# Performance work log

Hardware: AMD Instinct MI355X
Metric: run time of the kernel (lower is better)

## Reference

```python
import jax, jax.numpy as jnp
import numpy as np
from jax import lax

N, K = 4, 8
B, C, H, W = 16, 64, 256, 256


def setup_inputs() -> dict:
    key = jax.random.key(0)
    k1, k2, k3 = jax.random.split(key, 3)
    x = jax.random.normal(k1, (B, C, H, W), dtype=jnp.float32)
    z = jax.random.normal(k2, (B, C, N * K, N * K), dtype=jnp.float32)
    # torch init is ones; perturb slightly so the FFT filtering is non-trivial
    freq_coeff = 1.0 + 0.1 * jax.random.normal(k3, (K, K // 2 + 1, 2), dtype=jnp.float32)
    return {"x": x, "z": z, "freq_coeff": freq_coeff}


def _get_feature_weights(z, freq_coeff, n, k):
    b, c = z.shape[0], z.shape[1]
    # [b,c,n,k,n,k] -> [b,n,n,c,k,k] -> [b*n*n, c, k, k]
    w1 = z.reshape(b, c, n, k, n, k).transpose(0, 2, 4, 1, 3, 5).reshape(b * n * n, c, k, k)
    f = jnp.fft.rfft2(w1, norm="ortho")  # [b*n*n, c, k, k//2+1] complex
    # torch.rfft(..)*freq_coeff multiplies real/imag parts by separate real coeffs
    f_new = f.real * freq_coeff[..., 0] + 1j * (f.imag * freq_coeff[..., 1])
    return jnp.fft.irfft2(f_new, s=(k, k), norm="ortho")  # [b*n*n, c, k, k]


def _grouped_conv(data, weight, b):
    # data: [1, b*c, h, w], weight: [b*n*n, c, k, k], groups=b, stride 2, VALID
    return lax.conv_general_dilated(
        data, weight, window_strides=(2, 2), padding="VALID",
        dimension_numbers=("NCHW", "OIHW", "NCHW"), feature_group_count=b)


def reference(x, z, freq_coeff):
    k = freq_coeff.shape[0]
    n = z.shape[2] // k
    b, c, h, w = x.shape
    weight = _get_feature_weights(z, freq_coeff, n, k)
    data = x.reshape(1, b * c, h, w)
    resp = _grouped_conv(data, weight, b)  # [1, b*n*n, h', w']
    norm = _grouped_conv(data * data, jnp.ones_like(weight), b)
    norm = norm + jnp.std(norm, ddof=1) / 10 + 1e-9
    norm = lax.stop_gradient(0.01 / jnp.sqrt(norm))
    resp = resp * norm
    _, cc, hh, ww = resp.shape
    return resp.reshape(b, cc // b, hh, ww)
```

## Files before the change

### kernel.cpp

```cpp
#include <hip/hip_runtime.h>

typedef short short8 __attribute__((ext_vector_type(8)));
typedef float f32x4 __attribute__((ext_vector_type(4)));
typedef unsigned int uint4v __attribute__((ext_vector_type(4)));

static constexpr int OHW = 125;
static constexpr int PLN = OHW * OHW;

__device__ inline unsigned int bf16_rne(float f) {
  unsigned int u = __float_as_uint(f);
  return (u + 0x7FFFu + ((u >> 16) & 1u)) >> 16;
}

__global__ __launch_bounds__(256) void fft_mat_kernel(
    const float* __restrict__ fc, float* __restrict__ Mt, double* __restrict__ red) {
  if (blockIdx.x == 0 && threadIdx.x < 2) red[threadIdx.x] = 0.0;
  int e = blockIdx.x * 256 + threadIdx.x;
  int uv = e >> 6, xy = e & 63;
  int u = uv >> 3, v = uv & 7, xx = xy >> 3, yy = xy & 7;
  const float R2 = 0.70710678118654752f;
  const float ct[8] = {1.f, R2, 0.f, -R2, -1.f, -R2, 0.f, R2};
  const float st[8] = {0.f, R2, 1.f, R2, 0.f, -R2, -1.f, -R2};
  float sumv = 0.f;
  #pragma unroll
  for (int p = 0; p < 8; ++p) {
    #pragma unroll
    for (int q = 0; q < 8; ++q) {
      float Re, Im;
      if (q <= 4) {
        int th = (p * u + q * v) & 7;
        float a = fc[(p * 5 + q) * 2 + 0];
        float b = fc[(p * 5 + q) * 2 + 1];
        Re = a * ct[th];
        Im = -b * st[th];
      } else {
        int pp = (8 - p) & 7, qq = 8 - q;
        int th = (pp * u + qq * v) & 7;
        float a = fc[(pp * 5 + qq) * 2 + 0];
        float b = fc[(pp * 5 + qq) * 2 + 1];
        Re = a * ct[th];
        Im = b * st[th];
      }
      int ph = (p * xx + q * yy) & 7;
      sumv += Re * ct[ph] - Im * st[ph];
    }
  }
  Mt[e] = sumv * (1.0f / 64.0f);
}

__global__ __launch_bounds__(256) void weight_kernel(
    const float* __restrict__ z, const float* __restrict__ Mt,
    unsigned short* __restrict__ Wq) {
  int blk = blockIdx.x;
  int G = blk >> 2, cq = blk & 3;
  int b = G >> 4, n1 = (G >> 2) & 3, n2 = G & 3;
  int oc = G & 15;
  int tid = threadIdx.x;
  int cs = tid >> 6, xy = tid & 63;
  __shared__ float Ms[4096];
  __shared__ float zb[4][64];
  for (int i = tid; i < 4096; i += 256) Ms[i] = Mt[i];
  for (int it = 0; it < 4; ++it) {
    int c = cq * 16 + cs * 4 + it;
    __syncthreads();
    int u = xy >> 3, vv = xy & 7;
    zb[cs][xy] = z[(size_t)(b * 64 + c) * 1024 + (n1 * 8 + u) * 32 + (n2 * 8 + vv)];
    __syncthreads();
    float acc = 0.f;
    #pragma unroll
    for (int i = 0; i < 64; ++i) acc += Ms[i * 64 + xy] * zb[cs][i];
    Wq[((size_t)(b * 64 + c) * 16 + oc) * 64 + xy] = (unsigned short)bf16_rne(acc);
  }
}

__global__ __launch_bounds__(256) void conv_fused_kernel(
    const float* __restrict__ x, const unsigned short* __restrict__ Wq,
    float* __restrict__ resp, float* __restrict__ plane, double* __restrict__ red) {
  __shared__ unsigned int ldsx[2016];
  const int g = blockIdx.x, iblk = blockIdx.y, jh = blockIdx.z;
  const int i0 = iblk * 4;
  const int tid = threadIdx.x;
  const int lane = tid & 63, ri = tid >> 6;
  const int q = lane >> 4, n = lane & 15;

  const float* xg = x + (size_t)g * 64 * 65536;
  const unsigned short* wgc = Wq + (size_t)g * 65536;

  int it_goff[2], it_l[2];
  bool it_act[2];
  #pragma unroll
  for (int s = 0; s < 2; ++s) {
    int item = tid + (s << 8);
    int row = item / 36, c4 = item - row * 36;
    it_act[s] = row < 14;
    int rabs = 2 * i0 + row; if (rabs > 255) rabs = 255;
    int cabs = 128 * jh + 4 * c4; if (cabs > 252) cabs = 252;
    it_goff[s] = rabs * 256 + cabs;
    it_l[s] = row * 72 + 2 * c4;
  }
  const int aoff0 = n * 64 + q * 8;
  int dbase[2];
  #pragma unroll
  for (int h = 0; h < 2; ++h)
    dbase[h] = (2 * ri + q + 4 * h) * 72 + n;

  f32x4 acc[4];
  #pragma unroll
  for (int t = 0; t < 4; ++t) acc[t] = (f32x4){0.f, 0.f, 0.f, 0.f};
  float racc[2][2] = {{0.f, 0.f}, {0.f, 0.f}};

  f32x4 xv[2];
  short8 a_cur[2], a_nxt[2];

  #pragma unroll
  for (int s = 0; s < 2; ++s) xv[s] = *(const f32x4*)(xg + it_goff[s]);
  #pragma unroll
  for (int h = 0; h < 2; ++h)
    a_cur[h] = *(const short8*)(wgc + aoff0 + 32 * h);
  #pragma unroll
  for (int s = 0; s < 2; ++s) {
    if (it_act[s]) {
      racc[s][0] += xv[s][0] * xv[s][0] + xv[s][1] * xv[s][1];
      racc[s][1] += xv[s][2] * xv[s][2] + xv[s][3] * xv[s][3];
      unsigned int p0 = bf16_rne(xv[s][0]) | (bf16_rne(xv[s][1]) << 16);
      unsigned int p1 = bf16_rne(xv[s][2]) | (bf16_rne(xv[s][3]) << 16);
      ldsx[it_l[s]] = p0;
      ldsx[it_l[s] + 1] = p1;
    }
  }
  #pragma unroll
  for (int s = 0; s < 2; ++s) xv[s] = *(const f32x4*)(xg + 65536 + it_goff[s]);
  #pragma unroll
  for (int h = 0; h < 2; ++h)
    a_nxt[h] = *(const short8*)(wgc + 1024 + aoff0 + 32 * h);
  __syncthreads();

  for (int c = 0; c < 64; ++c) {
    int cb = c & 1;
    if (c < 63) {
      int bo = ((c + 1) & 1) * 1008;
      #pragma unroll
      for (int s = 0; s < 2; ++s) {
        if (it_act[s]) {
          racc[s][0] += xv[s][0] * xv[s][0] + xv[s][1] * xv[s][1];
          racc[s][1] += xv[s][2] * xv[s][2] + xv[s][3] * xv[s][3];
          unsigned int p0 = bf16_rne(xv[s][0]) | (bf16_rne(xv[s][1]) << 16);
          unsigned int p1 = bf16_rne(xv[s][2]) | (bf16_rne(xv[s][3]) << 16);
          ldsx[bo + it_l[s]] = p0;
          ldsx[bo + it_l[s] + 1] = p1;
        }
      }
      if (c < 62) {
        const float* xc = xg + (size_t)(c + 2) * 65536;
        #pragma unroll
        for (int s = 0; s < 2; ++s) xv[s] = *(const f32x4*)(xc + it_goff[s]);
      }
    }
    const unsigned int* xb = ldsx + cb * 1008;
    #pragma unroll
    for (int h = 0; h < 2; ++h) {
      short8 af = a_cur[h];
      int base = dbase[h];
      #pragma unroll
      for (int T = 0; T < 4; ++T) {
        int d = base + 16 * T;
        uint4v u;
        u.x = xb[d]; u.y = xb[d + 1]; u.z = xb[d + 2]; u.w = xb[d + 3];
        short8 bf = __builtin_bit_cast(short8, u);
        acc[T] = __builtin_amdgcn_mfma_f32_16x16x32_bf16(af, bf, acc[T], 0, 0, 0);
      }
    }
    a_cur[0] = a_nxt[0];
    a_cur[1] = a_nxt[1];
    if (c < 62) {
      const unsigned short* wc = wgc + (size_t)(c + 2) * 1024;
      #pragma unroll
      for (int h = 0; h < 2; ++h)
        a_nxt[h] = *(const short8*)(wc + aoff0 + 32 * h);
    }
    __syncthreads();
  }

  const int i = i0 + ri;
  if (i < OHW) {
    float* rbase = resp + (size_t)g * 16 * PLN + i * OHW;
    #pragma unroll
    for (int T = 0; T < 4; ++T) {
      int j = jh * 64 + T * 16 + n;
      if (j < OHW) {
        #pragma unroll
        for (int r = 0; r < 4; ++r) {
          int oc = q * 4 + r;
          rbase[(size_t)oc * PLN + j] = acc[T][r];
        }
      }
    }
  }

  float* Rl = (float*)ldsx;
  #pragma unroll
  for (int s = 0; s < 2; ++s) {
    if (it_act[s]) {
      Rl[it_l[s]] = racc[s][0];
      Rl[it_l[s] + 1] = racc[s][1];
    }
  }
  __syncthreads();

  int jl = lane;
  float nv = 0.f;
  #pragma unroll
  for (int r = 0; r < 8; ++r) {
    const float* Rr = Rl + (2 * ri + r) * 72 + jl;
    nv += Rr[0] + Rr[1] + Rr[2] + Rr[3];
  }
  int jj = jh * 64 + jl;
  double sv = 0.0, sv2 = 0.0;
  if (i < OHW && jj < OHW) {
    plane[(g * OHW + i) * OHW + jj] = nv;
    sv = (double)nv;
    sv2 = (double)nv * (double)nv;
  }
  #pragma unroll
  for (int off = 32; off > 0; off >>= 1) {
    sv += __shfl_down(sv, off);
    sv2 += __shfl_down(sv2, off);
  }
  __shared__ double sred[8];
  if (lane == 0) { sred[ri] = sv; sred[4 + ri] = sv2; }
  __syncthreads();
  if (tid == 0)
    atomicAdd(&red[0], sred[0] + sred[1] + sred[2] + sred[3]);
  if (tid == 64)
    atomicAdd(&red[1], sred[4] + sred[5] + sred[6] + sred[7]);
}

__global__ void finalize_kernel(const double* __restrict__ red, float* __restrict__ shiftp) {
  double sum = red[0], sumsq = red[1];
  double n = 256.0 * OHW * OHW;
  double mu = 16.0 * sum / n;
  double var = (16.0 * sumsq - n * mu * mu) / (n - 1.0);
  *shiftp = (float)(sqrt(var) / 10.0 + 1e-9);
}

__global__ __launch_bounds__(256) void scale_kernel(
    const float* __restrict__ resp, const float* __restrict__ plane,
    const float* __restrict__ shiftp, float* __restrict__ out) {
  int idx = blockIdx.x * 256 + threadIdx.x;
  float shift = *shiftp;
  int gp = idx / (16 * PLN);
  int rem = idx - gp * 16 * PLN;
  int ij = rem % PLN;
  float nv = plane[gp * PLN + ij];
  out[idx] = resp[idx] * 0.01f * rsqrtf(nv + shift);
}

extern "C" void kernel_launch(void* const* d_in, const int* in_sizes, int n_in,
                              void* d_out, int out_size, void* d_ws, size_t ws_size,
                              hipStream_t stream) {
  const float* x  = (const float*)d_in[0];
  const float* z  = (const float*)d_in[1];
  const float* fc = (const float*)d_in[2];
  float* out = (float*)d_out;

  char* ws = (char*)d_ws;
  unsigned short* Wq = (unsigned short*)(ws);
  float*  Mt     = (float*)(ws + 2097152);
  float*  resp   = (float*)(ws + 2113536);
  float*  plane  = (float*)(ws + 18113536);
  double* red    = (double*)(ws + 19113536);
  float*  shiftp = (float*)(ws + 19113552);

  fft_mat_kernel<<<16, 256, 0, stream>>>(fc, Mt, red);
  weight_kernel<<<1024, 256, 0, stream>>>(z, Mt, Wq);
  conv_fused_kernel<<<dim3(16, 32, 2), 256, 0, stream>>>(x, Wq, resp, plane, red);
  finalize_kernel<<<1, 1, 0, stream>>>(red, shiftp);
  scale_kernel<<<(16 * 16 * PLN) / 256, 256, 0, stream>>>(resp, plane, shiftp, out);
}
```

Baseline: 406.5 us.

## Double conv block height to 8 output rows with 512 threads; vectorize scale kernel

The conv kernel now computes 8 output rows per block with 8 wavefronts instead of 4 rows with 4 wavefronts. The staged input tile grows to 22 rows, so the overlapping input halo is loaded less often relative to useful work. The scale kernel processes four elements per thread with vector loads and stores. The larger blocks use more LDS and registers per block and halve the grid size, which can reduce occupancy and the number of blocks available to fill the device.

```diff
diff --git a/kernel.cpp b/kernel.cpp
--- a/kernel.cpp
+++ b/kernel.cpp
@@ -73,12 +73,17 @@
   }
 }
 
-__global__ __launch_bounds__(256) void conv_fused_kernel(
+static constexpr int SROWS = 22;
+static constexpr int SC4   = 34;
+static constexpr int LDW   = 72;
+static constexpr int LBUF  = SROWS * LDW;
+
+__global__ __launch_bounds__(512) void conv_fused_kernel(
     const float* __restrict__ x, const unsigned short* __restrict__ Wq,
     float* __restrict__ resp, float* __restrict__ plane, double* __restrict__ red) {
-  __shared__ unsigned int ldsx[2016];
+  __shared__ unsigned int ldsx[2 * LBUF];
   const int g = blockIdx.x, iblk = blockIdx.y, jh = blockIdx.z;
-  const int i0 = iblk * 4;
+  const int i0 = iblk * 8;
   const int tid = threadIdx.x;
   const int lane = tid & 63, ri = tid >> 6;
   const int q = lane >> 4, n = lane & 15;
@@ -90,19 +95,19 @@
   bool it_act[2];
   #pragma unroll
   for (int s = 0; s < 2; ++s) {
-    int item = tid + (s << 8);
-    int row = item / 36, c4 = item - row * 36;
-    it_act[s] = row < 14;
+    int item = tid + (s << 9);
+    int row = item / SC4, c4 = item - row * SC4;
+    it_act[s] = row < SROWS;
     int rabs = 2 * i0 + row; if (rabs > 255) rabs = 255;
     int cabs = 128 * jh + 4 * c4; if (cabs > 252) cabs = 252;
     it_goff[s] = rabs * 256 + cabs;
-    it_l[s] = row * 72 + 2 * c4;
+    it_l[s] = row * LDW + 2 * c4;
   }
   const int aoff0 = n * 64 + q * 8;
   int dbase[2];
   #pragma unroll
   for (int h = 0; h < 2; ++h)
-    dbase[h] = (2 * ri + q + 4 * h) * 72 + n;
+    dbase[h] = (2 * ri + q + 4 * h) * LDW + n;
 
   f32x4 acc[4];
   #pragma unroll
@@ -113,7 +118,8 @@
   short8 a_cur[2], a_nxt[2];
 
   #pragma unroll
-  for (int s = 0; s < 2; ++s) xv[s] = *(const f32x4*)(xg + it_goff[s]);
+  for (int s = 0; s < 2; ++s)
+    if (it_act[s]) xv[s] = *(const f32x4*)(xg + it_goff[s]);
   #pragma unroll
   for (int h = 0; h < 2; ++h)
     a_cur[h] = *(const short8*)(wgc + aoff0 + 32 * h);
@@ -129,7 +135,8 @@
     }
   }
   #pragma unroll
-  for (int s = 0; s < 2; ++s) xv[s] = *(const f32x4*)(xg + 65536 + it_goff[s]);
+  for (int s = 0; s < 2; ++s)
+    if (it_act[s]) xv[s] = *(const f32x4*)(xg + 65536 + it_goff[s]);
   #pragma unroll
   for (int h = 0; h < 2; ++h)
     a_nxt[h] = *(const short8*)(wgc + 1024 + aoff0 + 32 * h);
@@ -138,7 +145,7 @@
   for (int c = 0; c < 64; ++c) {
     int cb = c & 1;
     if (c < 63) {
-      int bo = ((c + 1) & 1) * 1008;
+      int bo = ((c + 1) & 1) * LBUF;
       #pragma unroll
       for (int s = 0; s < 2; ++s) {
         if (it_act[s]) {
@@ -153,10 +160,11 @@
       if (c < 62) {
         const float* xc = xg + (size_t)(c + 2) * 65536;
         #pragma unroll
-        for (int s = 0; s < 2; ++s) xv[s] = *(const f32x4*)(xc + it_goff[s]);
-      }
-    }
-    const unsigned int* xb = ldsx + cb * 1008;
+        for (int s = 0; s < 2; ++s)
+          if (it_act[s]) xv[s] = *(const f32x4*)(xc + it_goff[s]);
+      }
+    }
+    const unsigned int* xb = ldsx + cb * LBUF;
     #pragma unroll
     for (int h = 0; h < 2; ++h) {
       short8 af = a_cur[h];
@@ -211,7 +219,7 @@
   float nv = 0.f;
   #pragma unroll
   for (int r = 0; r < 8; ++r) {
-    const float* Rr = Rl + (2 * ri + r) * 72 + jl;
+    const float* Rr = Rl + (2 * ri + r) * LDW + jl;
     nv += Rr[0] + Rr[1] + Rr[2] + Rr[3];
   }
   int jj = jh * 64 + jl;
@@ -226,13 +234,15 @@
     sv += __shfl_down(sv, off);
     sv2 += __shfl_down(sv2, off);
   }
-  __shared__ double sred[8];
-  if (lane == 0) { sred[ri] = sv; sred[4 + ri] = sv2; }
+  __shared__ double sred[16];
+  if (lane == 0) { sred[ri] = sv; sred[8 + ri] = sv2; }
   __syncthreads();
   if (tid == 0)
-    atomicAdd(&red[0], sred[0] + sred[1] + sred[2] + sred[3]);
+    atomicAdd(&red[0], sred[0] + sred[1] + sred[2] + sred[3] +
+                       sred[4] + sred[5] + sred[6] + sred[7]);
   if (tid == 64)
-    atomicAdd(&red[1], sred[4] + sred[5] + sred[6] + sred[7]);
+    atomicAdd(&red[1], sred[8] + sred[9] + sred[10] + sred[11] +
+                       sred[12] + sred[13] + sred[14] + sred[15]);
 }
 
 __global__ void finalize_kernel(const double* __restrict__ red, float* __restrict__ shiftp) {
@@ -246,13 +256,22 @@
 __global__ __launch_bounds__(256) void scale_kernel(
     const float* __restrict__ resp, const float* __restrict__ plane,
     const float* __restrict__ shiftp, float* __restrict__ out) {
-  int idx = blockIdx.x * 256 + threadIdx.x;
+  int t = blockIdx.x * 256 + threadIdx.x;
+  int idx0 = t * 4;
+  if (idx0 >= 16 * 16 * PLN) return;
   float shift = *shiftp;
-  int gp = idx / (16 * PLN);
-  int rem = idx - gp * 16 * PLN;
-  int ij = rem % PLN;
-  float nv = plane[gp * PLN + ij];
-  out[idx] = resp[idx] * 0.01f * rsqrtf(nv + shift);
+  int gp = idx0 / (16 * PLN);
+  int rem = idx0 - gp * (16 * PLN);
+  int ij0 = rem % PLN;
+  f32x4 r = *(const f32x4*)(resp + idx0);
+  const float* pl = plane + (size_t)gp * PLN;
+  f32x4 o;
+  #pragma unroll
+  for (int k = 0; k < 4; ++k) {
+    int ij = ij0 + k; if (ij >= PLN) ij -= PLN;
+    o[k] = r[k] * 0.01f * rsqrtf(pl[ij] + shift);
+  }
+  *(f32x4*)(out + idx0) = o;
 }
 
 extern "C" void kernel_launch(void* const* d_in, const int* in_sizes, int n_in,
@@ -273,7 +292,7 @@
 
   fft_mat_kernel<<<16, 256, 0, stream>>>(fc, Mt, red);
   weight_kernel<<<1024, 256, 0, stream>>>(z, Mt, Wq);
-  conv_fused_kernel<<<dim3(16, 32, 2), 256, 0, stream>>>(x, Wq, resp, plane, red);
+  conv_fused_kernel<<<dim3(16, 16, 2), 512, 0, stream>>>(x, Wq, resp, plane, red);
   finalize_kernel<<<1, 1, 0, stream>>>(red, shiftp);
-  scale_kernel<<<(16 * 16 * PLN) / 256, 256, 0, stream>>>(resp, plane, shiftp, out);
-}
+  scale_kernel<<<(16 * 16 * PLN / 4 + 255) / 256, 256, 0, stream>>>(resp, plane, shiftp, out);
+}
```

Result: faster. 397.5 us (-2.2%).
